# Optimization experiments

Hardware: AMD Instinct MI355X
Metric: run time of the kernel (lower is better)

The kernel has to match this reference:

```python
import jax, jax.numpy as jnp
import numpy as np

TOPOLOGY = [0,0,1,2,3,4,0,6,7,8,0,10,11,12,12,14,15,16,12,18,19,20]
J = len(TOPOLOGY)          # 22 joints
POS, OFF = 3, 1            # position_feature, offset_feature
CIN = (POS + OFF) * J      # 88 conv channels


def _adj():
    # adj[parent, child] = 1 (root skipped), fixed skeleton adjacency
    a = np.zeros((J, J), np.float32)
    for i, p in enumerate(TOPOLOGY):
        if i:
            a[p, i] = 1.0
    return jnp.asarray(a)


def setup_inputs() -> dict:
    key = jax.random.key(0)
    ks = jax.random.split(key, 32)

    def n(k, shape, s):
        return jax.random.normal(k, shape, dtype=jnp.float32) * s

    inp = {
        "input": jax.random.normal(ks[0], (128, 2048, J, POS), dtype=jnp.float32),
        "offset": jax.random.normal(ks[1], (128, 2048, J, OFF), dtype=jnp.float32),
    }
    i = 2
    for c in ("conv1", "conv2", "conv3"):
        inp[c + "_w"] = n(ks[i], (CIN, CIN, 4), 0.05); i += 1  # OIH
        inp[c + "_b"] = jnp.zeros((CIN,), jnp.float32)
    for g in ("g1", "g2"):
        inp[g + "_n2n_w"] = n(ks[i], (POS, POS), 0.3); i += 1
        inp[g + "_n2n_b"] = jnp.zeros((POS,), jnp.float32)
        inp[g + "_e2n_we"] = n(ks[i], (OFF, POS), 0.3); i += 1
        inp[g + "_e2n_wn"] = n(ks[i], (POS, POS), 0.3); i += 1
        inp[g + "_e2n_b"] = jnp.zeros((POS,), jnp.float32)
        inp[g + "_n2e_wn"] = n(ks[i], (POS, OFF), 0.3); i += 1
        inp[g + "_n2e_we"] = n(ks[i], (OFF, OFF), 0.3); i += 1
        inp[g + "_n2e_b"] = jnp.zeros((OFF,), jnp.float32)
        inp[g + "_lin_w"] = n(ks[i], (2 * POS, POS), 0.3); i += 1
        inp[g + "_lin_b"] = jnp.zeros((POS,), jnp.float32)
    return inp


def _conv_block(x, off, w, b):
    # concat node+edge feats, fold (joint, feature) into channels, temporal Conv1d k=4 s=2 p=1
    x = jnp.concatenate([x, off], axis=-1)          # [B,F,J,C]
    B, F, Jn, C = x.shape
    y = x.transpose(0, 2, 3, 1).reshape(B, Jn * C, F)
    y = jax.lax.conv_general_dilated(y, w, window_strides=(2,), padding=[(1, 1)],
                                     dimension_numbers=("NCH", "OIH", "NCH"))
    y = y + b[None, :, None]
    Fn = y.shape[-1]                                # F // 2
    return y.transpose(0, 2, 1).reshape(B, Fn, Jn, C)


def _graph_block(x, A, n2n_w, n2n_b, e2n_we, e2n_wn, e2n_b,
                 n2e_wn, n2e_we, n2e_b, lin_w, lin_b):
    node, edge = x[..., :POS], x[..., POS:]
    # adjacency broadcast (torch code replicated it B*F times; same math)
    agg_n = jnp.einsum('ij,bfjc->bfic', A, node)
    agg_e = jnp.einsum('ij,bfjc->bfic', A, edge)
    f1 = agg_n @ n2n_w + n2n_b                              # Node2Node
    f2 = agg_e @ e2n_we + node @ e2n_wn + e2n_b             # Edge2Node
    new_edge = jnp.einsum('ji,bfjc->bfic', A, node) @ n2e_wn + edge @ n2e_we + n2e_b  # Node2Edge
    h = jnp.concatenate([f1, f2], axis=-1) @ lin_w + lin_b  # fuse 2*c_out_node -> c_out_node
    return h, new_edge


def reference(input, offset,
              conv1_w, conv1_b, conv2_w, conv2_b, conv3_w, conv3_b,
              g1_n2n_w, g1_n2n_b, g1_e2n_we, g1_e2n_wn, g1_e2n_b,
              g1_n2e_wn, g1_n2e_we, g1_n2e_b, g1_lin_w, g1_lin_b,
              g2_n2n_w, g2_n2n_b, g2_e2n_we, g2_e2n_wn, g2_e2n_b,
              g2_n2e_wn, g2_n2e_we, g2_n2e_b, g2_lin_w, g2_lin_b):
    A = _adj()
    x = _conv_block(input, offset, conv1_w, conv1_b)
    x, off = _graph_block(x, A, g1_n2n_w, g1_n2n_b, g1_e2n_we, g1_e2n_wn, g1_e2n_b,
                          g1_n2e_wn, g1_n2e_we, g1_n2e_b, g1_lin_w, g1_lin_b)
    x = _conv_block(x, off, conv2_w, conv2_b)
    x, off = _graph_block(x, A, g2_n2n_w, g2_n2n_b, g2_e2n_we, g2_e2n_wn, g2_e2n_b,
                          g2_n2e_wn, g2_n2e_we, g2_n2e_b, g2_lin_w, g2_lin_b)
    x = _conv_block(x, off, conv3_w, conv3_b)
    return x[..., :POS]   # final slice when last dim != c_out_node
```

## Files before the change

kernel.cpp:

```cpp
#include <hip/hip_runtime.h>


static constexpr int Jn   = 22;
static constexpr int C4   = 88;
static constexpr int KK   = 352;
static constexpr int NPAD = 96;
static constexpr int LROW = 104;
static constexpr int YROW = 101;
static constexpr int NFR  = 130;

typedef __attribute__((ext_vector_type(8))) short    short8;
typedef __attribute__((ext_vector_type(4))) float    floatx4;
typedef __attribute__((ext_vector_type(4))) unsigned uintx4;

__device__ constexpr int TOPc[Jn] = {0,0,1,2,3,4,0,6,7,8,0,10,11,12,12,14,15,16,12,18,19,20};

__device__ __forceinline__ unsigned short f2bf(float f) {
    unsigned u = __builtin_bit_cast(unsigned, f);
    unsigned r = (u + 0x7FFFu + ((u >> 16) & 1u)) >> 16;
    return (unsigned short)r;
}

struct GW {
    const float *n2n_w, *n2n_b, *e2n_we, *e2n_wn, *e2n_b;
    const float *n2e_wn, *n2e_we, *n2e_b, *lin_w, *lin_b;
};

__global__ __launch_bounds__(256)
void prep_weights(const float* __restrict__ w1, const float* __restrict__ w2,
                  const float* __restrict__ w3, unsigned short* __restrict__ o)
{
    const int i = blockIdx.x * 256 + threadIdx.x;
    constexpr int per = NPAD * KK;
    if (i >= 3 * per) return;
    const int s  = i / per, r = i - s * per;
    const int co = r / KK, k = r - co * KK;
    const int tap = k / C4, ci = k - tap * C4;
    const float* w = (s == 0) ? w1 : (s == 1) ? w2 : w3;
    const float v = (co < C4) ? w[((size_t)co * C4 + ci) * 4 + tap] : 0.f;
    o[i] = f2bf(v);
}

template<int FIN, int INM, int OUTM>
__global__ __launch_bounds__(256, 4)
void conv_fused(const float* __restrict__ xf, const float* __restrict__ xoff,
                const unsigned short* __restrict__ xbf,
                const unsigned short* __restrict__ wbf, const float* __restrict__ bias,
                void* __restrict__ yout, GW g)
{
    constexpr int FOUT   = FIN / 2;
    constexpr int NTILE  = FOUT / 64;
    __shared__ __align__(16) unsigned char smem[NFR * LROW * 2];
    unsigned short* Xs = reinterpret_cast<unsigned short*>(smem);
    float*          Yt = reinterpret_cast<float*>(smem);

    const int tid = threadIdx.x;
    const int b   = blockIdx.x / NTILE;
    const int fo0 = (blockIdx.x - b * NTILE) * 64;
    const int gf0 = 2 * fo0 - 1;

    if (INM == 0) {
        for (int idx = tid; idx < NFR * 66; idx += 256) {
            const int lf = idx / 66, p = idx - lf * 66;
            const int gf = gf0 + lf;
            const int gfc = min(max(gf, 0), FIN - 1);
            float v = xf[((size_t)b * FIN + gfc) * 66 + p];
            v = (gf == gfc) ? v : 0.f;
            Xs[lf * LROW + p + p / 3] = f2bf(v);
        }
        for (int idx = tid; idx < NFR * 22; idx += 256) {
            const int lf = idx / 22, j = idx - lf * 22;
            const int gf = gf0 + lf;
            const int gfc = min(max(gf, 0), FIN - 1);
            float v = xoff[((size_t)b * FIN + gfc) * 22 + j];
            v = (gf == gfc) ? v : 0.f;
            Xs[lf * LROW + 4 * j + 3] = f2bf(v);
        }
    } else {
        const uintx4 zero = {0u, 0u, 0u, 0u};
        for (int idx = tid; idx < NFR * 11; idx += 256) {
            const int lf = idx / 11, q = idx - lf * 11;
            const int gf = gf0 + lf;
            const int gfc = min(max(gf, 0), FIN - 1);
            uintx4 v = *reinterpret_cast<const uintx4*>(xbf + ((size_t)b * FIN + gfc) * C4 + q * 8);
            v = (gf == gfc) ? v : zero;
            *reinterpret_cast<uintx4*>(Xs + lf * LROW + q * 8) = v;
        }
    }
    __syncthreads();

    const int wid = tid >> 6, lane = tid & 63;
    const int l15 = lane & 15, h = lane >> 4;
    const int mhalf = wid >> 1, nhalf = wid & 1;

    floatx4 acc[2][3];
#pragma unroll
    for (int mt = 0; mt < 2; ++mt)
#pragma unroll
        for (int nti = 0; nti < 3; ++nti)
            acc[mt][nti] = (floatx4){0.f, 0.f, 0.f, 0.f};

    const unsigned short* wb = wbf + (size_t)(nhalf * 48 + l15) * KK;

#pragma unroll
    for (int kt = 0; kt < 11; ++kt) {
        const int q   = 4 * kt + h;
        const int tap = (unsigned)q / 11u;
        const int ci0 = 8 * (q - 11 * tap);
        const int lfb = 2 * l15 + tap;

        short8 afr[2];
#pragma unroll
        for (int mt = 0; mt < 2; ++mt)
            afr[mt] = *reinterpret_cast<const short8*>(
                Xs + (mhalf * 64 + mt * 32 + lfb) * LROW + ci0);

        short8 bfr[3];
#pragma unroll
        for (int nti = 0; nti < 3; ++nti)
            bfr[nti] = *reinterpret_cast<const short8*>(wb + (size_t)nti * 16 * KK + kt * 32 + 8 * h);

#pragma unroll
        for (int mt = 0; mt < 2; ++mt)
#pragma unroll
            for (int nti = 0; nti < 3; ++nti)
                acc[mt][nti] = __builtin_amdgcn_mfma_f32_16x16x32_bf16(
                    afr[mt], bfr[nti], acc[mt][nti], 0, 0, 0);
    }

    if (OUTM == 1) {
        float* yo = reinterpret_cast<float*>(yout);
#pragma unroll
        for (int mt = 0; mt < 2; ++mt)
#pragma unroll
            for (int nti = 0; nti < 3; ++nti) {
                const int co = nhalf * 48 + nti * 16 + l15;
                if (co < C4) {
                    const int j = co >> 2, c = co & 3;
                    if (c < 3) {
                        const float bi = bias[co];
#pragma unroll
                        for (int r = 0; r < 4; ++r) {
                            const int m = fo0 + mhalf * 32 + mt * 16 + 4 * h + r;
                            yo[((size_t)(b * FOUT + m) * Jn + j) * 3 + c] = acc[mt][nti][r] + bi;
                        }
                    }
                }
            }
        return;
    }

    __syncthreads();
#pragma unroll
    for (int mt = 0; mt < 2; ++mt)
#pragma unroll
        for (int nti = 0; nti < 3; ++nti) {
            const int co = nhalf * 48 + nti * 16 + l15;
            const float bi = (co < C4) ? bias[co] : 0.f;
#pragma unroll
            for (int r = 0; r < 4; ++r) {
                const int row = mhalf * 32 + mt * 16 + 4 * h + r;
                Yt[row * YROW + co] = acc[mt][nti][r] + bi;
            }
        }
    __syncthreads();

    {
        const int row = tid & 63, grp = tid >> 6;
        const float* yr = Yt + row * YROW;

        float n2n[9], n2nb[3], e2we[3], e2wn[9], e2nb[3], newn[3], lin[18], linb[3];
#pragma unroll
        for (int i = 0; i < 9;  ++i) n2n[i]  = g.n2n_w[i];
#pragma unroll
        for (int i = 0; i < 3;  ++i) n2nb[i] = g.n2n_b[i];
#pragma unroll
        for (int i = 0; i < 3;  ++i) e2we[i] = g.e2n_we[i];
#pragma unroll
        for (int i = 0; i < 9;  ++i) e2wn[i] = g.e2n_wn[i];
#pragma unroll
        for (int i = 0; i < 3;  ++i) e2nb[i] = g.e2n_b[i];
#pragma unroll
        for (int i = 0; i < 3;  ++i) newn[i] = g.n2e_wn[i];
        const float newe = g.n2e_we[0];
        const float neb  = g.n2e_b[0];
#pragma unroll
        for (int i = 0; i < 18; ++i) lin[i]  = g.lin_w[i];
#pragma unroll
        for (int i = 0; i < 3;  ++i) linb[i] = g.lin_b[i];

        unsigned short* xout = reinterpret_cast<unsigned short*>(yout);
        const size_t orow = ((size_t)b * FOUT + fo0 + row) * C4;

#pragma unroll
        for (int i = 0; i < Jn; ++i) {
            if (i / 6 != grp) continue;
            float an0 = 0.f, an1 = 0.f, an2 = 0.f, ae = 0.f;
#pragma unroll
            for (int j = 1; j < Jn; ++j) {
                if (TOPc[j] == i) {
                    an0 += yr[4 * j]; an1 += yr[4 * j + 1];
                    an2 += yr[4 * j + 2]; ae += yr[4 * j + 3];
                }
            }
            const float s0 = yr[4 * i], s1 = yr[4 * i + 1], s2 = yr[4 * i + 2], se = yr[4 * i + 3];
            float f1[3], f2[3];
#pragma unroll
            for (int c = 0; c < 3; ++c) {
                f1[c] = an0 * n2n[c] + an1 * n2n[3 + c] + an2 * n2n[6 + c] + n2nb[c];
                f2[c] = ae * e2we[c] + s0 * e2wn[c] + s1 * e2wn[3 + c] + s2 * e2wn[6 + c] + e2nb[c];
            }
            float p0 = 0.f, p1 = 0.f, p2 = 0.f;
            if (i > 0) {
                const int p = TOPc[i];
                p0 = yr[4 * p]; p1 = yr[4 * p + 1]; p2 = yr[4 * p + 2];
            }
            const float ne = p0 * newn[0] + p1 * newn[1] + p2 * newn[2] + se * newe + neb;

            float o[3];
#pragma unroll
            for (int c = 0; c < 3; ++c)
                o[c] = f1[0] * lin[0 + c] + f1[1] * lin[3 + c] + f1[2] * lin[6 + c]
                     + f2[0] * lin[9 + c] + f2[1] * lin[12 + c] + f2[2] * lin[15 + c] + linb[c];

            uint2 pk;
            pk.x = (unsigned)f2bf(o[0]) | ((unsigned)f2bf(o[1]) << 16);
            pk.y = (unsigned)f2bf(o[2]) | ((unsigned)f2bf(ne)   << 16);
            *reinterpret_cast<uint2*>(xout + orow + 4 * i) = pk;
        }
    }
}

extern "C" void kernel_launch(void* const* d_in, const int* in_sizes, int n_in,
                              void* d_out, int out_size, void* d_ws, size_t ws_size,
                              hipStream_t stream)
{
    (void)n_in; (void)out_size; (void)ws_size;

    const float* input  = (const float*)d_in[0];
    const float* offset = (const float*)d_in[1];
    const float* c1w = (const float*)d_in[2]; const float* c1b = (const float*)d_in[3];
    const float* c2w = (const float*)d_in[4]; const float* c2b = (const float*)d_in[5];
    const float* c3w = (const float*)d_in[6]; const float* c3b = (const float*)d_in[7];

    GW g1 { (const float*)d_in[8],  (const float*)d_in[9],  (const float*)d_in[10],
            (const float*)d_in[11], (const float*)d_in[12], (const float*)d_in[13],
            (const float*)d_in[14], (const float*)d_in[15], (const float*)d_in[16],
            (const float*)d_in[17] };
    GW g2 { (const float*)d_in[18], (const float*)d_in[19], (const float*)d_in[20],
            (const float*)d_in[21], (const float*)d_in[22], (const float*)d_in[23],
            (const float*)d_in[24], (const float*)d_in[25], (const float*)d_in[26],
            (const float*)d_in[27] };

    const int B = in_sizes[0] / (2048 * Jn * 3);

    unsigned short* wbf = (unsigned short*)d_ws;
    unsigned short* X1  = wbf + (size_t)3 * NPAD * KK;
    unsigned short* X2  = X1 + (size_t)B * 1024 * C4;

    {
        const int tot = 3 * NPAD * KK;
        prep_weights<<<(tot + 255) / 256, 256, 0, stream>>>(c1w, c2w, c3w, wbf);
    }

    conv_fused<2048, 0, 0><<<B * 16, 256, 0, stream>>>(input, offset, nullptr,
                                                       wbf, c1b, X1, g1);
    conv_fused<1024, 1, 0><<<B * 8, 256, 0, stream>>>(nullptr, nullptr, X1,
                                                      wbf + NPAD * KK, c2b, X2, g2);
    conv_fused<512, 1, 1><<<B * 4, 256, 0, stream>>>(nullptr, nullptr, X2,
                                                     wbf + 2 * NPAD * KK, c3b, d_out, g2);
}
```

Baseline: 84.06 us.

## Permute channel layout to node-then-edge order for contiguous vectorized loads and stores

Measured after the change: 90.68 us. 7.9% more time.

```diff
diff --git a/kernel.cpp b/kernel.cpp
--- a/kernel.cpp
+++ b/kernel.cpp
@@ -20,6 +20,9 @@
     unsigned r = (u + 0x7FFFu + ((u >> 16) & 1u)) >> 16;
     return (unsigned short)r;
 }
+__device__ __forceinline__ int qmap(int q) {
+    return (q < 66) ? 4 * (q / 3) + (q % 3) : 4 * (q - 66) + 3;
+}
 
 struct GW {
     const float *n2n_w, *n2n_b, *e2n_we, *e2n_wn, *e2n_b;
@@ -28,17 +31,27 @@
 
 __global__ __launch_bounds__(256)
 void prep_weights(const float* __restrict__ w1, const float* __restrict__ w2,
-                  const float* __restrict__ w3, unsigned short* __restrict__ o)
+                  const float* __restrict__ w3,
+                  const float* __restrict__ b1, const float* __restrict__ b2,
+                  const float* __restrict__ b3,
+                  unsigned short* __restrict__ wo, float* __restrict__ bo)
 {
     const int i = blockIdx.x * 256 + threadIdx.x;
     constexpr int per = NPAD * KK;
-    if (i >= 3 * per) return;
-    const int s  = i / per, r = i - s * per;
-    const int co = r / KK, k = r - co * KK;
-    const int tap = k / C4, ci = k - tap * C4;
-    const float* w = (s == 0) ? w1 : (s == 1) ? w2 : w3;
-    const float v = (co < C4) ? w[((size_t)co * C4 + ci) * 4 + tap] : 0.f;
-    o[i] = f2bf(v);
+    if (i < 3 * per) {
+        const int s = i / per, r = i - s * per;
+        const int co = r / KK, k = r - co * KK;
+        const int tap = k / C4, q = k - tap * C4;
+        const float* w = (s == 0) ? w1 : (s == 1) ? w2 : w3;
+        float v = 0.f;
+        if (co < C4) v = w[((size_t)qmap(co) * C4 + qmap(q)) * 4 + tap];
+        wo[i] = f2bf(v);
+    } else if (i < 3 * per + 3 * NPAD) {
+        const int j = i - 3 * per;
+        const int s = j / NPAD, q = j - s * NPAD;
+        const float* bb = (s == 0) ? b1 : (s == 1) ? b2 : b3;
+        bo[j] = (q < C4) ? bb[qmap(q)] : 0.f;
+    }
 }
 
 template<int FIN, int INM, int OUTM>
@@ -48,8 +61,8 @@
                 const unsigned short* __restrict__ wbf, const float* __restrict__ bias,
                 void* __restrict__ yout, GW g)
 {
-    constexpr int FOUT   = FIN / 2;
-    constexpr int NTILE  = FOUT / 64;
+    constexpr int FOUT  = FIN / 2;
+    constexpr int NTILE = FOUT / 64;
     __shared__ __align__(16) unsigned char smem[NFR * LROW * 2];
     unsigned short* Xs = reinterpret_cast<unsigned short*>(smem);
     float*          Yt = reinterpret_cast<float*>(smem);
@@ -59,32 +72,53 @@
     const int fo0 = (blockIdx.x - b * NTILE) * 64;
     const int gf0 = 2 * fo0 - 1;
 
-    if (INM == 0) {
-        for (int idx = tid; idx < NFR * 66; idx += 256) {
-            const int lf = idx / 66, p = idx - lf * 66;
-            const int gf = gf0 + lf;
-            const int gfc = min(max(gf, 0), FIN - 1);
-            float v = xf[((size_t)b * FIN + gfc) * 66 + p];
-            v = (gf == gfc) ? v : 0.f;
-            Xs[lf * LROW + p + p / 3] = f2bf(v);
-        }
-        for (int idx = tid; idx < NFR * 22; idx += 256) {
-            const int lf = idx / 22, j = idx - lf * 22;
-            const int gf = gf0 + lf;
-            const int gfc = min(max(gf, 0), FIN - 1);
-            float v = xoff[((size_t)b * FIN + gfc) * 22 + j];
-            v = (gf == gfc) ? v : 0.f;
-            Xs[lf * LROW + 4 * j + 3] = f2bf(v);
-        }
-    } else {
-        const uintx4 zero = {0u, 0u, 0u, 0u};
-        for (int idx = tid; idx < NFR * 11; idx += 256) {
-            const int lf = idx / 11, q = idx - lf * 11;
-            const int gf = gf0 + lf;
-            const int gfc = min(max(gf, 0), FIN - 1);
-            uintx4 v = *reinterpret_cast<const uintx4*>(xbf + ((size_t)b * FIN + gfc) * C4 + q * 8);
-            v = (gf == gfc) ? v : zero;
-            *reinterpret_cast<uintx4*>(Xs + lf * LROW + q * 8) = v;
+    {
+        const int fgrp = tid >> 1, gg = tid & 1;
+#pragma unroll
+        for (int cc = 0; cc < 2; ++cc) {
+            const int lf = cc * 128 + fgrp;
+            if (lf < NFR) {
+                const int gf  = gf0 + lf;
+                const int gfc = min(max(gf, 0), FIN - 1);
+                const bool inb = (gf == gfc);
+                unsigned short* dst = Xs + lf * LROW;
+                if (INM == 0) {
+                    const float2* srcN = reinterpret_cast<const float2*>(xf + ((size_t)b * FIN + gfc) * 66);
+                    const float2* srcE = reinterpret_cast<const float2*>(xoff + ((size_t)b * FIN + gfc) * 22);
+#pragma unroll
+                    for (int i2 = 0; i2 < 17; ++i2) {
+                        const int idx = 2 * i2 + gg;
+                        if (idx < 33) {
+                            const float2 v = srcN[idx];
+                            unsigned pk = (unsigned)f2bf(v.x) | ((unsigned)f2bf(v.y) << 16);
+                            pk = inb ? pk : 0u;
+                            *reinterpret_cast<unsigned*>(dst + 2 * idx) = pk;
+                        }
+                    }
+#pragma unroll
+                    for (int i2 = 0; i2 < 6; ++i2) {
+                        const int idx = 2 * i2 + gg;
+                        if (idx < 11) {
+                            const float2 v = srcE[idx];
+                            unsigned pk = (unsigned)f2bf(v.x) | ((unsigned)f2bf(v.y) << 16);
+                            pk = inb ? pk : 0u;
+                            *reinterpret_cast<unsigned*>(dst + 66 + 2 * idx) = pk;
+                        }
+                    }
+                } else {
+                    const uintx4* src = reinterpret_cast<const uintx4*>(xbf + ((size_t)b * FIN + gfc) * C4);
+                    const uintx4 zero = {0u, 0u, 0u, 0u};
+#pragma unroll
+                    for (int i2 = 0; i2 < 6; ++i2) {
+                        const int idx = 2 * i2 + gg;
+                        if (idx < 11) {
+                            uintx4 v = src[idx];
+                            if (!inb) v = zero;
+                            *reinterpret_cast<uintx4*>(dst + 8 * idx) = v;
+                        }
+                    }
+                }
+            }
         }
     }
     __syncthreads();
@@ -135,15 +169,12 @@
 #pragma unroll
             for (int nti = 0; nti < 3; ++nti) {
                 const int co = nhalf * 48 + nti * 16 + l15;
-                if (co < C4) {
-                    const int j = co >> 2, c = co & 3;
-                    if (c < 3) {
-                        const float bi = bias[co];
-#pragma unroll
-                        for (int r = 0; r < 4; ++r) {
-                            const int m = fo0 + mhalf * 32 + mt * 16 + 4 * h + r;
-                            yo[((size_t)(b * FOUT + m) * Jn + j) * 3 + c] = acc[mt][nti][r] + bi;
-                        }
+                if (co < 66) {
+                    const float bi = bias[co];
+#pragma unroll
+                    for (int r = 0; r < 4; ++r) {
+                        const int m = fo0 + mhalf * 32 + mt * 16 + 4 * h + r;
+                        yo[(size_t)(b * FOUT + m) * 66 + co] = acc[mt][nti][r] + bi;
                     }
                 }
             }
@@ -156,7 +187,7 @@
 #pragma unroll
         for (int nti = 0; nti < 3; ++nti) {
             const int co = nhalf * 48 + nti * 16 + l15;
-            const float bi = (co < C4) ? bias[co] : 0.f;
+            const float bi = bias[co];
 #pragma unroll
             for (int r = 0; r < 4; ++r) {
                 const int row = mhalf * 32 + mt * 16 + 4 * h + r;
@@ -199,11 +230,11 @@
 #pragma unroll
             for (int j = 1; j < Jn; ++j) {
                 if (TOPc[j] == i) {
-                    an0 += yr[4 * j]; an1 += yr[4 * j + 1];
-                    an2 += yr[4 * j + 2]; ae += yr[4 * j + 3];
+                    an0 += yr[3 * j]; an1 += yr[3 * j + 1];
+                    an2 += yr[3 * j + 2]; ae += yr[66 + j];
                 }
             }
-            const float s0 = yr[4 * i], s1 = yr[4 * i + 1], s2 = yr[4 * i + 2], se = yr[4 * i + 3];
+            const float s0 = yr[3 * i], s1 = yr[3 * i + 1], s2 = yr[3 * i + 2], se = yr[66 + i];
             float f1[3], f2[3];
 #pragma unroll
             for (int c = 0; c < 3; ++c) {
@@ -213,7 +244,7 @@
             float p0 = 0.f, p1 = 0.f, p2 = 0.f;
             if (i > 0) {
                 const int p = TOPc[i];
-                p0 = yr[4 * p]; p1 = yr[4 * p + 1]; p2 = yr[4 * p + 2];
+                p0 = yr[3 * p]; p1 = yr[3 * p + 1]; p2 = yr[3 * p + 2];
             }
             const float ne = p0 * newn[0] + p1 * newn[1] + p2 * newn[2] + se * newe + neb;
 
@@ -223,10 +254,10 @@
                 o[c] = f1[0] * lin[0 + c] + f1[1] * lin[3 + c] + f1[2] * lin[6 + c]
                      + f2[0] * lin[9 + c] + f2[1] * lin[12 + c] + f2[2] * lin[15 + c] + linb[c];
 
-            uint2 pk;
-            pk.x = (unsigned)f2bf(o[0]) | ((unsigned)f2bf(o[1]) << 16);
-            pk.y = (unsigned)f2bf(o[2]) | ((unsigned)f2bf(ne)   << 16);
-            *reinterpret_cast<uint2*>(xout + orow + 4 * i) = pk;
+            xout[orow + 3 * i]     = f2bf(o[0]);
+            xout[orow + 3 * i + 1] = f2bf(o[1]);
+            xout[orow + 3 * i + 2] = f2bf(o[2]);
+            xout[orow + 66 + i]    = f2bf(ne);
         }
     }
 }
@@ -255,18 +286,19 @@
     const int B = in_sizes[0] / (2048 * Jn * 3);
 
     unsigned short* wbf = (unsigned short*)d_ws;
-    unsigned short* X1  = wbf + (size_t)3 * NPAD * KK;
-    unsigned short* X2  = X1 + (size_t)B * 1024 * C4;
+    float* pb = (float*)(wbf + (size_t)3 * NPAD * KK);
+    unsigned short* X1 = (unsigned short*)(pb + 3 * NPAD);
+    unsigned short* X2 = X1 + (size_t)B * 1024 * C4;
 
     {
-        const int tot = 3 * NPAD * KK;
-        prep_weights<<<(tot + 255) / 256, 256, 0, stream>>>(c1w, c2w, c3w, wbf);
+        const int tot = 3 * NPAD * KK + 3 * NPAD;
+        prep_weights<<<(tot + 255) / 256, 256, 0, stream>>>(c1w, c2w, c3w, c1b, c2b, c3b, wbf, pb);
     }
 
     conv_fused<2048, 0, 0><<<B * 16, 256, 0, stream>>>(input, offset, nullptr,
-                                                       wbf, c1b, X1, g1);
+                                                       wbf, pb, X1, g1);
     conv_fused<1024, 1, 0><<<B * 8, 256, 0, stream>>>(nullptr, nullptr, X1,
-                                                      wbf + NPAD * KK, c2b, X2, g2);
+                                                      wbf + NPAD * KK, pb + NPAD, X2, g2);
     conv_fused<512, 1, 1><<<B * 4, 256, 0, stream>>>(nullptr, nullptr, X2,
-                                                     wbf + 2 * NPAD * KK, c3b, d_out, g2);
-}
+                                                     wbf + 2 * NPAD * KK, pb + 2 * NPAD, d_out, g2);
+}
```
